# Optimization experiments

Measured on AMD Instinct MI355X. Metric: run time of the kernel, lower is better.

## Reference

```python
import jax, jax.numpy as jnp
import numpy as np

NUM_NODES = 512
HEADS = 4
IN_F = 256
OUT_F = 128
EPS = 1e-5


def _layernorm(x, g, b):
    mu = jnp.mean(x, axis=-1, keepdims=True)
    var = jnp.mean(jnp.square(x - mu), axis=-1, keepdims=True)
    return (x - mu) * jax.lax.rsqrt(var + EPS) * g + b


def setup_inputs() -> dict:
    key = jax.random.key(0)
    ks = jax.random.split(key, 16)
    N = 32 * NUM_NODES
    E = 262144
    s = 0.05
    return {
        "x": jax.random.normal(ks[0], (N, IN_F), jnp.float32),
        "edge_index": jax.random.randint(ks[1], (2, E), 0, N, jnp.int64),
        "W_l": jax.random.normal(ks[2], (IN_F, HEADS * OUT_F), jnp.float32) * s,
        "W_r": jax.random.normal(ks[3], (IN_F, HEADS * OUT_F), jnp.float32) * s,
        "att": jax.random.normal(ks[4], (HEADS, OUT_F), jnp.float32) * s,
        "gat_bias": jnp.zeros((OUT_F,), jnp.float32),
        "gat_gamma": jnp.ones((OUT_F,), jnp.float32),
        "gat_beta": jnp.zeros((OUT_F,), jnp.float32),
        "cnn_W": jax.random.normal(ks[5], (IN_F, OUT_F), jnp.float32) * s,
        "cnn_b": jnp.zeros((OUT_F,), jnp.float32),
        "conv_W": jax.random.normal(ks[6], (OUT_F, OUT_F, 7), jnp.float32) * s,
        "conv_b": jnp.zeros((OUT_F,), jnp.float32),
        "cnn_gamma": jnp.ones((OUT_F,), jnp.float32),
        "cnn_beta": jnp.zeros((OUT_F,), jnp.float32),
        "res_W": jax.random.normal(ks[7], (IN_F, OUT_F), jnp.float32) * s,
        "res_b": jnp.zeros((OUT_F,), jnp.float32),
        "fuse_gamma": jnp.ones((OUT_F,), jnp.float32),
        "fuse_beta": jnp.zeros((OUT_F,), jnp.float32),
    }


def reference(x, edge_index, W_l, W_r, att, gat_bias, gat_gamma, gat_beta,
              cnn_W, cnn_b, conv_W, conv_b, cnn_gamma, cnn_beta,
              res_W, res_b, fuse_gamma, fuse_beta):
    N = x.shape[0]
    B = N // NUM_NODES
    # --- GATv2 branch (add self-loops like PyG default) ---
    loop = jnp.arange(N, dtype=edge_index.dtype)
    src = jnp.concatenate([edge_index[0], loop])
    dst = jnp.concatenate([edge_index[1], loop])
    x_l = (x @ W_l).reshape(N, HEADS, OUT_F)
    x_r = (x @ W_r).reshape(N, HEADS, OUT_F)
    e = x_l[src] + x_r[dst]                      # [E+N, H, F]
    e = jnp.where(e > 0, e, 0.2 * e)             # leaky_relu, slope 0.2
    score = jnp.einsum('ehf,hf->eh', e, att)     # [E+N, H]
    m = jax.ops.segment_max(score, dst, num_segments=N)
    ex = jnp.exp(score - m[dst])
    denom = jax.ops.segment_sum(ex, dst, num_segments=N)
    alpha = ex / denom[dst]
    agg = jax.ops.segment_sum(alpha[:, :, None] * x_l[src], dst, num_segments=N)
    h_gat = jnp.mean(agg, axis=1) + gat_bias     # concat=False -> head mean
    h_gat = jnp.where(h_gat > 0, h_gat, 0.01 * h_gat)  # nn.LeakyReLU default
    h_gat = _layernorm(h_gat, gat_gamma, gat_beta)
    # --- CNN branch ---
    xc = x @ cnn_W + cnn_b                       # [N, F]
    xc = xc.reshape(B, NUM_NODES, OUT_F).transpose(0, 2, 1)  # [B, F, L]
    hc = jax.lax.conv_general_dilated(xc, conv_W, window_strides=(1,),
                                      padding=[(3, 3)],
                                      dimension_numbers=('NCW', 'OIW', 'NCW'))
    hc = hc + conv_b[None, :, None]
    hc = hc.transpose(0, 2, 1).reshape(N, OUT_F)
    hc = jax.nn.relu(hc)
    hc = _layernorm(hc, cnn_gamma, cnn_beta)
    # --- fuse + residual ---
    h = h_gat + hc + (x @ res_W + res_b)
    return _layernorm(h, fuse_gamma, fuse_beta)
```

## Files before the change

kernel.cpp:

```cpp
#include <hip/hip_runtime.h>
#include <hip/hip_bf16.h>
#include <math.h>

#define IN_F 256
#define OUT_F 128
#define HEADS 4
#define HF 512
#define NCAT 1280

typedef __hip_bfloat16 bf16;
typedef unsigned short ushort_t;

using bf16x8 = __attribute__((ext_vector_type(8))) short;
using f32x4  = __attribute__((ext_vector_type(4))) float;

__device__ __forceinline__ float bflo(unsigned u) { return __uint_as_float(u << 16); }
__device__ __forceinline__ float bfhi(unsigned u) { return __uint_as_float(u & 0xffff0000u); }
__device__ __forceinline__ float bf2f(ushort_t u) { return __uint_as_float((unsigned)u << 16); }
__device__ __forceinline__ ushort_t f2bf(float f) {
    __hip_bfloat16 h = __float2bfloat16(f);
    return *reinterpret_cast<ushort_t*>(&h);
}

template <int CTRL>
__device__ __forceinline__ float dpp_add(float s) {
    int t = __builtin_amdgcn_update_dpp(0, __float_as_int(s), CTRL, 0xf, 0xf, true);
    return s + __int_as_float(t);
}
__device__ __forceinline__ float rowsum16(float s) {
    s = dpp_add<0x121>(s);
    s = dpp_add<0x122>(s);
    s = dpp_add<0x124>(s);
    s = dpp_add<0x128>(s);
    return s;
}

__global__ __launch_bounds__(256) void cvt_x_kernel(
    const float* __restrict__ x, ushort_t* __restrict__ xb, int n) {
    int i = (blockIdx.x * 256 + threadIdx.x) * 8;
    if (i >= n) return;
    float4 a = *(const float4*)(x + i);
    float4 b = *(const float4*)(x + i + 4);
    uint4 o;
    o.x = f2bf(a.x) | ((unsigned)f2bf(a.y) << 16);
    o.y = f2bf(a.z) | ((unsigned)f2bf(a.w) << 16);
    o.z = f2bf(b.x) | ((unsigned)f2bf(b.y) << 16);
    o.w = f2bf(b.z) | ((unsigned)f2bf(b.w) << 16);
    *(uint4*)(xb + i) = o;
}

__global__ __launch_bounds__(256) void build_weights_kernel(
    const float* __restrict__ Wl, const float* __restrict__ Wr,
    const float* __restrict__ Wc, const float* __restrict__ Wres,
    const float* __restrict__ Wconv,
    ushort_t* __restrict__ Wt, ushort_t* __restrict__ Wt2) {
    int idx = blockIdx.x * 256 + threadIdx.x;
    if (idx < NCAT * 256) {
        int n = idx >> 8, k = idx & 255;
        float v;
        if (n < 512)       v = Wl[(size_t)k * 512 + n];
        else if (n < 1024) v = Wr[(size_t)k * 512 + (n - 512)];
        else if (n < 1152) v = Wc[(size_t)k * 128 + (n - 1024)];
        else               v = Wres[(size_t)k * 128 + (n - 1152)];
        Wt[idx] = f2bf(v);
    } else {
        int j = idx - NCAT * 256;
        if (j < 7 * 128 * 128) {
            int k = j >> 14, o = (j >> 7) & 127, i = j & 127;
            Wt2[j] = f2bf(Wconv[((size_t)o * 128 + i) * 7 + k]);
        }
    }
}

__global__ __launch_bounds__(256) void mfma_gemm(
    const ushort_t* __restrict__ A,
    const ushort_t* __restrict__ Wt,
    ushort_t* __restrict__ xlb, ushort_t* __restrict__ xrb,
    ushort_t* __restrict__ xcb, ushort_t* __restrict__ resb,
    int M) {
    __shared__ ushort_t As[128][40];
    __shared__ ushort_t Bs[128][40];
    int tid = threadIdx.x;
    int lane = tid & 63, wid = tid >> 6;
    int wr = (wid >> 1) * 64, wc = (wid & 1) * 64;
    int brow = blockIdx.y * 128, bcol = blockIdx.x * 128;
    f32x4 acc[4][4] = {};
    int kb = (lane >> 4) * 8;
    int rl = lane & 15;
    for (int k0 = 0; k0 < 256; k0 += 32) {
        #pragma unroll
        for (int i = 0; i < 2; ++i) {
            int idx = tid + 256 * i;
            int row = idx >> 2, seg = idx & 3;
            *(uint4*)&As[row][seg * 8] =
                *(const uint4*)(A + (size_t)(brow + row) * 256 + k0 + seg * 8);
            *(uint4*)&Bs[row][seg * 8] =
                *(const uint4*)(Wt + (size_t)(bcol + row) * 256 + k0 + seg * 8);
        }
        __syncthreads();
        bf16x8 af[4], bfr[4];
        #pragma unroll
        for (int m = 0; m < 4; ++m) af[m] = *(const bf16x8*)&As[wr + m * 16 + rl][kb];
        #pragma unroll
        for (int n = 0; n < 4; ++n) bfr[n] = *(const bf16x8*)&Bs[wc + n * 16 + rl][kb];
        #pragma unroll
        for (int m = 0; m < 4; ++m)
            #pragma unroll
            for (int n = 0; n < 4; ++n)
                acc[m][n] = __builtin_amdgcn_mfma_f32_16x16x32_bf16(
                    af[m], bfr[n], acc[m][n], 0, 0, 0);
        __syncthreads();
    }
    ushort_t* dstp; int cstride, cb;
    if (bcol < 512)       { dstp = xlb;  cstride = 512; cb = bcol; }
    else if (bcol < 1024) { dstp = xrb;  cstride = 512; cb = bcol - 512; }
    else if (bcol < 1152) { dstp = xcb;  cstride = 128; cb = bcol - 1024; }
    else                  { dstp = resb; cstride = 128; cb = bcol - 1152; }
    int rowb = (lane >> 4) * 4;
    #pragma unroll
    for (int m = 0; m < 4; ++m)
        #pragma unroll
        for (int n = 0; n < 4; ++n) {
            int col = cb + wc + n * 16 + rl;
            #pragma unroll
            for (int q = 0; q < 4; ++q) {
                int row = brow + wr + m * 16 + rowb + q;
                dstp[(size_t)row * cstride + col] = f2bf(acc[m][n][q]);
            }
        }
}

__global__ __launch_bounds__(256) void conv_mfma(
    const ushort_t* __restrict__ xcb, const float* __restrict__ cnn_b,
    const ushort_t* __restrict__ Wt2, float* __restrict__ hc) {
    __shared__ ushort_t As[70][136];
    __shared__ ushort_t Bs[128][136];
    int tid = threadIdx.x;
    int lane = tid & 63, wid = tid >> 6;
    int wr = (wid >> 1) * 32, wc = (wid & 1) * 64;
    int b = blockIdx.y, l0 = blockIdx.x * 64;
    for (int u = tid; u < 70 * 16; u += 256) {
        int r = u >> 4, seg = u & 15;
        int l = l0 - 3 + r;
        uint4 o4 = make_uint4(0, 0, 0, 0);
        if (l >= 0 && l < 512) {
            uint4 v = *(const uint4*)(xcb + (size_t)(b * 512 + l) * 128 + seg * 8);
            float4 b0 = *(const float4*)(cnn_b + seg * 8);
            float4 b1 = *(const float4*)(cnn_b + seg * 8 + 4);
            o4.x = f2bf(bflo(v.x) + b0.x) | ((unsigned)f2bf(bfhi(v.x) + b0.y) << 16);
            o4.y = f2bf(bflo(v.y) + b0.z) | ((unsigned)f2bf(bfhi(v.y) + b0.w) << 16);
            o4.z = f2bf(bflo(v.z) + b1.x) | ((unsigned)f2bf(bfhi(v.z) + b1.y) << 16);
            o4.w = f2bf(bflo(v.w) + b1.z) | ((unsigned)f2bf(bfhi(v.w) + b1.w) << 16);
        }
        *(uint4*)&As[r][seg * 8] = o4;
    }
    f32x4 acc[2][4] = {};
    int rl = lane & 15, kb = (lane >> 4) * 8;
    for (int k = 0; k < 7; ++k) {
        __syncthreads();
        for (int u = tid; u < 128 * 16; u += 256) {
            int r = u >> 4, seg = u & 15;
            *(uint4*)&Bs[r][seg * 8] =
                *(const uint4*)(Wt2 + ((size_t)(k * 128 + r)) * 128 + seg * 8);
        }
        __syncthreads();
        #pragma unroll
        for (int kk = 0; kk < 4; ++kk) {
            bf16x8 af[2], bfr[4];
            af[0] = *(const bf16x8*)&As[wr + 0  + rl + k][kk * 32 + kb];
            af[1] = *(const bf16x8*)&As[wr + 16 + rl + k][kk * 32 + kb];
            #pragma unroll
            for (int n = 0; n < 4; ++n)
                bfr[n] = *(const bf16x8*)&Bs[wc + n * 16 + rl][kk * 32 + kb];
            #pragma unroll
            for (int m = 0; m < 2; ++m)
                #pragma unroll
                for (int n = 0; n < 4; ++n)
                    acc[m][n] = __builtin_amdgcn_mfma_f32_16x16x32_bf16(
                        af[m], bfr[n], acc[m][n], 0, 0, 0);
        }
    }
    int rowb = (lane >> 4) * 4;
    #pragma unroll
    for (int m = 0; m < 2; ++m)
        #pragma unroll
        for (int n = 0; n < 4; ++n) {
            int col = wc + n * 16 + rl;
            #pragma unroll
            for (int q = 0; q < 4; ++q) {
                int l = l0 + wr + m * 16 + rowb + q;
                hc[(size_t)(b * 512 + l) * 128 + col] = acc[m][n][q];
            }
        }
}

__global__ __launch_bounds__(256) void hist_kernel(
    const int* __restrict__ ei, int* __restrict__ counts, int E) {
    int e = blockIdx.x * 256 + threadIdx.x;
    if (e < E) atomicAdd(&counts[ei[E + e]], 1);
}

__global__ __launch_bounds__(1024) void scan_kernel(
    const int* __restrict__ counts, int* __restrict__ offs,
    int* __restrict__ cursor, int N) {
    __shared__ int wsum[16];
    int t = threadIdx.x;
    int lane = t & 63, w = t >> 6;
    int base = t * 16;
    int local[16], s = 0;
    #pragma unroll
    for (int i = 0; i < 16; ++i) {
        int v = (base + i < N) ? counts[base + i] : 0;
        local[i] = v; s += v;
    }
    int sc = s;
    #pragma unroll
    for (int off = 1; off < 64; off <<= 1) {
        int v = __shfl_up(sc, off);
        if (lane >= off) sc += v;
    }
    if (lane == 63) wsum[w] = sc;
    __syncthreads();
    if (w == 0 && lane < 16) {
        int v = wsum[lane];
        int scv = v;
        #pragma unroll
        for (int off = 1; off < 16; off <<= 1) {
            int u = __shfl_up(scv, off);
            if (lane >= off) scv += u;
        }
        wsum[lane] = scv - v;
    }
    __syncthreads();
    int run = wsum[w] + sc - s;
    #pragma unroll
    for (int i = 0; i < 16; ++i) {
        if (base + i < N) { offs[base + i] = run; cursor[base + i] = run; }
        run += local[i];
    }
}

__global__ __launch_bounds__(256) void scatter_kernel(
    const int* __restrict__ ei, int* __restrict__ cursor,
    int* __restrict__ srcs, int E) {
    int e = blockIdx.x * 256 + threadIdx.x;
    if (e < E) {
        int d = ei[E + e];
        int p = atomicAdd(&cursor[d], 1);
        srcs[p] = ei[e];
    }
}

__global__ __launch_bounds__(256) void gat_fused_kernel(
    const ushort_t* __restrict__ xlb, const ushort_t* __restrict__ xrb,
    const int* __restrict__ srcs, const int* __restrict__ offs,
    const float* __restrict__ att, const float* __restrict__ gat_bias,
    const float* __restrict__ gat_gamma, const float* __restrict__ gat_beta,
    float* __restrict__ hgat_ln, int E, int N) {
    int wid = (blockIdx.x * 256 + threadIdx.x) >> 6;
    int lane = threadIdx.x & 63;
    if (wid >= N) return;
    int d = wid;
    const uint4 rv = ((const uint4*)(xrb + (size_t)d * HF))[lane];
    float xr8[8];
    xr8[0] = bflo(rv.x); xr8[1] = bfhi(rv.x);
    xr8[2] = bflo(rv.y); xr8[3] = bfhi(rv.y);
    xr8[4] = bflo(rv.z); xr8[5] = bfhi(rv.z);
    xr8[6] = bflo(rv.w); xr8[7] = bfhi(rv.w);
    const float4 a0 = ((const float4*)att)[lane * 2];
    const float4 a1 = ((const float4*)att)[lane * 2 + 1];
    const float aw[8] = {a0.x, a0.y, a0.z, a0.w, a1.x, a1.y, a1.z, a1.w};
    float acc[8] = {};
    float dn = 0.f;

    auto process = [&](uint4 lv) {
        float xl8[8];
        xl8[0] = bflo(lv.x); xl8[1] = bfhi(lv.x);
        xl8[2] = bflo(lv.y); xl8[3] = bfhi(lv.y);
        xl8[4] = bflo(lv.z); xl8[5] = bfhi(lv.z);
        xl8[6] = bflo(lv.w); xl8[7] = bfhi(lv.w);
        float s = 0.f;
        #pragma unroll
        for (int j = 0; j < 8; ++j) {
            float v = xl8[j] + xr8[j];
            v = v > 0.f ? v : 0.2f * v;
            s = fmaf(v, aw[j], s);
        }
        s = rowsum16(s);
        float ex = __expf(s);
        dn += ex;
        #pragma unroll
        for (int j = 0; j < 8; ++j) acc[j] = fmaf(ex, xl8[j], acc[j]);
    };

    process(((const uint4*)(xlb + (size_t)d * HF))[lane]);

    int start = offs[d];
    int end = (d == N - 1) ? E : offs[d + 1];
    int p = start;
    for (; p + 3 < end; p += 4) {
        int s0 = srcs[p], s1 = srcs[p + 1], s2 = srcs[p + 2], s3 = srcs[p + 3];
        uint4 l0 = ((const uint4*)(xlb + (size_t)s0 * HF))[lane];
        uint4 l1 = ((const uint4*)(xlb + (size_t)s1 * HF))[lane];
        uint4 l2 = ((const uint4*)(xlb + (size_t)s2 * HF))[lane];
        uint4 l3 = ((const uint4*)(xlb + (size_t)s3 * HF))[lane];
        process(l0); process(l1); process(l2); process(l3);
    }
    for (; p < end; ++p)
        process(((const uint4*)(xlb + (size_t)srcs[p] * HF))[lane]);

    float inv = 1.f / dn;
    float v[8];
    #pragma unroll
    for (int j = 0; j < 8; ++j) {
        float t2 = acc[j] * inv;
        t2 += __shfl_xor(t2, 16);
        t2 += __shfl_xor(t2, 32);
        v[j] = t2;
    }
    int h = lane >> 4;
    int col = (lane & 15) * 8 + 2 * h;
    float g0 = 0.25f * v[2 * h]     + gat_bias[col];
    float g1 = 0.25f * v[2 * h + 1] + gat_bias[col + 1];
    g0 = g0 > 0.f ? g0 : 0.01f * g0;
    g1 = g1 > 0.f ? g1 : 0.01f * g1;
    float s = g0 + g1;
    #pragma unroll
    for (int off = 32; off; off >>= 1) s += __shfl_xor(s, off);
    float mu = s * (1.f / 128.f);
    float d0 = g0 - mu, d1 = g1 - mu;
    float vs = d0 * d0 + d1 * d1;
    #pragma unroll
    for (int off = 32; off; off >>= 1) vs += __shfl_xor(vs, off);
    float rinv = rsqrtf(vs * (1.f / 128.f) + 1e-5f);
    hgat_ln[(size_t)d * 128 + col]     = d0 * rinv * gat_gamma[col]     + gat_beta[col];
    hgat_ln[(size_t)d * 128 + col + 1] = d1 * rinv * gat_gamma[col + 1] + gat_beta[col + 1];
}

__global__ __launch_bounds__(256) void final_ln_kernel(
    const float* __restrict__ hgat_ln, const float* __restrict__ hc,
    const ushort_t* __restrict__ resb, const float* __restrict__ conv_b,
    const float* __restrict__ cnn_gamma, const float* __restrict__ cnn_beta,
    const float* __restrict__ res_b, const float* __restrict__ fuse_gamma,
    const float* __restrict__ fuse_beta, float* __restrict__ out, int N) {
    int wid = (blockIdx.x * 256 + threadIdx.x) >> 6;
    int lane = threadIdx.x & 63;
    if (wid >= N) return;
    size_t base = (size_t)wid * 128;
    float h0 = fmaxf(hc[base + lane]      + conv_b[lane], 0.f);
    float h1 = fmaxf(hc[base + lane + 64] + conv_b[lane + 64], 0.f);
    float s = h0 + h1;
    #pragma unroll
    for (int off = 32; off; off >>= 1) s += __shfl_xor(s, off);
    float mu = s * (1.f / 128.f);
    float d0 = h0 - mu, d1 = h1 - mu;
    float vs = d0 * d0 + d1 * d1;
    #pragma unroll
    for (int off = 32; off; off >>= 1) vs += __shfl_xor(vs, off);
    float inv = rsqrtf(vs * (1.f / 128.f) + 1e-5f);
    float hcn0 = d0 * inv * cnn_gamma[lane]      + cnn_beta[lane];
    float hcn1 = d1 * inv * cnn_gamma[lane + 64] + cnn_beta[lane + 64];
    float v0 = hgat_ln[base + lane]      + hcn0
             + bf2f(resb[base + lane])      + res_b[lane];
    float v1 = hgat_ln[base + lane + 64] + hcn1
             + bf2f(resb[base + lane + 64]) + res_b[lane + 64];
    s = v0 + v1;
    #pragma unroll
    for (int off = 32; off; off >>= 1) s += __shfl_xor(s, off);
    mu = s * (1.f / 128.f);
    d0 = v0 - mu; d1 = v1 - mu;
    vs = d0 * d0 + d1 * d1;
    #pragma unroll
    for (int off = 32; off; off >>= 1) vs += __shfl_xor(vs, off);
    inv = rsqrtf(vs * (1.f / 128.f) + 1e-5f);
    out[base + lane]      = d0 * inv * fuse_gamma[lane]      + fuse_beta[lane];
    out[base + lane + 64] = d1 * inv * fuse_gamma[lane + 64] + fuse_beta[lane + 64];
}

extern "C" void kernel_launch(void* const* d_in, const int* in_sizes, int n_in,
                              void* d_out, int out_size, void* d_ws, size_t ws_size,
                              hipStream_t stream) {
    const float* x         = (const float*)d_in[0];
    const int*   ei        = (const int*)d_in[1];
    const float* W_l       = (const float*)d_in[2];
    const float* W_r       = (const float*)d_in[3];
    const float* att       = (const float*)d_in[4];
    const float* gat_bias  = (const float*)d_in[5];
    const float* gat_gamma = (const float*)d_in[6];
    const float* gat_beta  = (const float*)d_in[7];
    const float* cnn_W     = (const float*)d_in[8];
    const float* cnn_b     = (const float*)d_in[9];
    const float* conv_W    = (const float*)d_in[10];
    const float* conv_b    = (const float*)d_in[11];
    const float* cnn_gamma = (const float*)d_in[12];
    const float* cnn_beta  = (const float*)d_in[13];
    const float* res_W     = (const float*)d_in[14];
    const float* res_b     = (const float*)d_in[15];
    const float* fuse_gamma= (const float*)d_in[16];
    const float* fuse_beta = (const float*)d_in[17];

    int N = in_sizes[0] / IN_F;
    int E = in_sizes[1] / 2;

    char* ws = (char*)d_ws;
    size_t off = 0;
    ushort_t* xb     = (ushort_t*)(ws + off); off += (size_t)N * IN_F * 2;
    ushort_t* Wt     = (ushort_t*)(ws + off); off += (size_t)NCAT * IN_F * 2;
    ushort_t* Wt2    = (ushort_t*)(ws + off); off += (size_t)7 * 128 * 128 * 2;
    ushort_t* xlb    = (ushort_t*)(ws + off); off += (size_t)N * HF * 2;
    ushort_t* xrb    = (ushort_t*)(ws + off); off += (size_t)N * HF * 2;
    ushort_t* xcb    = (ushort_t*)(ws + off); off += (size_t)N * 128 * 2;
    ushort_t* resb   = (ushort_t*)(ws + off); off += (size_t)N * 128 * 2;
    int*  counts     = (int*)(ws + off);  off += (size_t)N * 4;
    int*  offs       = (int*)(ws + off);  off += (size_t)N * 4;
    int*  cursor     = (int*)(ws + off);  off += (size_t)N * 4;
    int*  srcs       = (int*)(ws + off);  off += (size_t)E * 4;
    float* hgat_ln   = (float*)(ws + off); off += (size_t)N * 128 * 4;
    float* hc        = (float*)(ws + off); off += (size_t)N * 128 * 4;

    hipMemsetAsync(counts, 0, (size_t)N * 4, stream);

    dim3 blk(256);
    hist_kernel<<<(E + 255) / 256, blk, 0, stream>>>(ei, counts, E);
    scan_kernel<<<1, 1024, 0, stream>>>(counts, offs, cursor, N);
    scatter_kernel<<<(E + 255) / 256, blk, 0, stream>>>(ei, cursor, srcs, E);

    cvt_x_kernel<<<(N * IN_F / 8 + 255) / 256, blk, 0, stream>>>(x, xb, N * IN_F);
    build_weights_kernel<<<(NCAT * 256 + 7 * 128 * 128 + 255) / 256, blk, 0, stream>>>(
        W_l, W_r, cnn_W, res_W, conv_W, Wt, Wt2);

    mfma_gemm<<<dim3(NCAT / 128, N / 128), blk, 0, stream>>>(
        xb, Wt, xlb, xrb, xcb, resb, N);

    gat_fused_kernel<<<(N + 3) / 4, blk, 0, stream>>>(
        xlb, xrb, srcs, offs, att, gat_bias, gat_gamma, gat_beta, hgat_ln, E, N);

    conv_mfma<<<dim3(8, 32), blk, 0, stream>>>(xcb, cnn_b, Wt2, hc);

    final_ln_kernel<<<(N + 3) / 4, blk, 0, stream>>>(
        hgat_ln, hc, resb, conv_b, cnn_gamma, cnn_beta, res_b,
        fuse_gamma, fuse_beta, (float*)d_out, N);
}
```

Before: 160.2 us.

## Merge prep kernels and fuse conv with final layernorm epilogue

Three small prep kernels (x bf16 conversion, weight packing, edge-degree histogram) become one launch that dispatches on block index. The conv MFMA kernel now uses 32-row tiles and applies bias, ReLU, both layernorms and the residual add in its epilogue via shared memory, so the fp32 hc intermediate and the separate final kernel are gone. Leaky-ReLU in the GAT score is rewritten as 0.6*v + 0.4*|v| to avoid a branch. The conv grid doubles and the weight tile is reloaded more often per output row, which costs some reuse in exchange for fewer launches and less global traffic.

```diff
diff --git a/kernel.cpp b/kernel.cpp
--- a/kernel.cpp
+++ b/kernel.cpp
@@ -35,40 +35,46 @@
     return s;
 }
 
-__global__ __launch_bounds__(256) void cvt_x_kernel(
-    const float* __restrict__ x, ushort_t* __restrict__ xb, int n) {
-    int i = (blockIdx.x * 256 + threadIdx.x) * 8;
-    if (i >= n) return;
-    float4 a = *(const float4*)(x + i);
-    float4 b = *(const float4*)(x + i + 4);
-    uint4 o;
-    o.x = f2bf(a.x) | ((unsigned)f2bf(a.y) << 16);
-    o.y = f2bf(a.z) | ((unsigned)f2bf(a.w) << 16);
-    o.z = f2bf(b.x) | ((unsigned)f2bf(b.y) << 16);
-    o.w = f2bf(b.z) | ((unsigned)f2bf(b.w) << 16);
-    *(uint4*)(xb + i) = o;
-}
-
-__global__ __launch_bounds__(256) void build_weights_kernel(
+__global__ __launch_bounds__(256) void prep_kernel(
+    const float* __restrict__ x, ushort_t* __restrict__ xb, int n_cvt,
     const float* __restrict__ Wl, const float* __restrict__ Wr,
     const float* __restrict__ Wc, const float* __restrict__ Wres,
     const float* __restrict__ Wconv,
-    ushort_t* __restrict__ Wt, ushort_t* __restrict__ Wt2) {
-    int idx = blockIdx.x * 256 + threadIdx.x;
-    if (idx < NCAT * 256) {
-        int n = idx >> 8, k = idx & 255;
-        float v;
-        if (n < 512)       v = Wl[(size_t)k * 512 + n];
-        else if (n < 1024) v = Wr[(size_t)k * 512 + (n - 512)];
-        else if (n < 1152) v = Wc[(size_t)k * 128 + (n - 1024)];
-        else               v = Wres[(size_t)k * 128 + (n - 1152)];
-        Wt[idx] = f2bf(v);
+    ushort_t* __restrict__ Wt, ushort_t* __restrict__ Wt2,
+    const int* __restrict__ ei, int* __restrict__ counts, int E,
+    int g1, int g2) {
+    int b = blockIdx.x;
+    if (b < g1) {
+        int i = (b * 256 + threadIdx.x) * 8;
+        if (i >= n_cvt) return;
+        float4 a = *(const float4*)(x + i);
+        float4 c = *(const float4*)(x + i + 4);
+        uint4 o;
+        o.x = f2bf(a.x) | ((unsigned)f2bf(a.y) << 16);
+        o.y = f2bf(a.z) | ((unsigned)f2bf(a.w) << 16);
+        o.z = f2bf(c.x) | ((unsigned)f2bf(c.y) << 16);
+        o.w = f2bf(c.z) | ((unsigned)f2bf(c.w) << 16);
+        *(uint4*)(xb + i) = o;
+    } else if (b < g2) {
+        int idx = (b - g1) * 256 + threadIdx.x;
+        if (idx < NCAT * 256) {
+            int n = idx >> 8, k = idx & 255;
+            float v;
+            if (n < 512)       v = Wl[(size_t)k * 512 + n];
+            else if (n < 1024) v = Wr[(size_t)k * 512 + (n - 512)];
+            else if (n < 1152) v = Wc[(size_t)k * 128 + (n - 1024)];
+            else               v = Wres[(size_t)k * 128 + (n - 1152)];
+            Wt[idx] = f2bf(v);
+        } else {
+            int j = idx - NCAT * 256;
+            if (j < 7 * 128 * 128) {
+                int k = j >> 14, o = (j >> 7) & 127, i = j & 127;
+                Wt2[j] = f2bf(Wconv[((size_t)o * 128 + i) * 7 + k]);
+            }
+        }
     } else {
-        int j = idx - NCAT * 256;
-        if (j < 7 * 128 * 128) {
-            int k = j >> 14, o = (j >> 7) & 127, i = j & 127;
-            Wt2[j] = f2bf(Wconv[((size_t)o * 128 + i) * 7 + k]);
-        }
+        int e = (b - g2) * 256 + threadIdx.x;
+        if (e < E) atomicAdd(&counts[ei[E + e]], 1);
     }
 }
 
@@ -128,76 +134,6 @@
                 dstp[(size_t)row * cstride + col] = f2bf(acc[m][n][q]);
             }
         }
-}
-
-__global__ __launch_bounds__(256) void conv_mfma(
-    const ushort_t* __restrict__ xcb, const float* __restrict__ cnn_b,
-    const ushort_t* __restrict__ Wt2, float* __restrict__ hc) {
-    __shared__ ushort_t As[70][136];
-    __shared__ ushort_t Bs[128][136];
-    int tid = threadIdx.x;
-    int lane = tid & 63, wid = tid >> 6;
-    int wr = (wid >> 1) * 32, wc = (wid & 1) * 64;
-    int b = blockIdx.y, l0 = blockIdx.x * 64;
-    for (int u = tid; u < 70 * 16; u += 256) {
-        int r = u >> 4, seg = u & 15;
-        int l = l0 - 3 + r;
-        uint4 o4 = make_uint4(0, 0, 0, 0);
-        if (l >= 0 && l < 512) {
-            uint4 v = *(const uint4*)(xcb + (size_t)(b * 512 + l) * 128 + seg * 8);
-            float4 b0 = *(const float4*)(cnn_b + seg * 8);
-            float4 b1 = *(const float4*)(cnn_b + seg * 8 + 4);
-            o4.x = f2bf(bflo(v.x) + b0.x) | ((unsigned)f2bf(bfhi(v.x) + b0.y) << 16);
-            o4.y = f2bf(bflo(v.y) + b0.z) | ((unsigned)f2bf(bfhi(v.y) + b0.w) << 16);
-            o4.z = f2bf(bflo(v.z) + b1.x) | ((unsigned)f2bf(bfhi(v.z) + b1.y) << 16);
-            o4.w = f2bf(bflo(v.w) + b1.z) | ((unsigned)f2bf(bfhi(v.w) + b1.w) << 16);
-        }
-        *(uint4*)&As[r][seg * 8] = o4;
-    }
-    f32x4 acc[2][4] = {};
-    int rl = lane & 15, kb = (lane >> 4) * 8;
-    for (int k = 0; k < 7; ++k) {
-        __syncthreads();
-        for (int u = tid; u < 128 * 16; u += 256) {
-            int r = u >> 4, seg = u & 15;
-            *(uint4*)&Bs[r][seg * 8] =
-                *(const uint4*)(Wt2 + ((size_t)(k * 128 + r)) * 128 + seg * 8);
-        }
-        __syncthreads();
-        #pragma unroll
-        for (int kk = 0; kk < 4; ++kk) {
-            bf16x8 af[2], bfr[4];
-            af[0] = *(const bf16x8*)&As[wr + 0  + rl + k][kk * 32 + kb];
-            af[1] = *(const bf16x8*)&As[wr + 16 + rl + k][kk * 32 + kb];
-            #pragma unroll
-            for (int n = 0; n < 4; ++n)
-                bfr[n] = *(const bf16x8*)&Bs[wc + n * 16 + rl][kk * 32 + kb];
-            #pragma unroll
-            for (int m = 0; m < 2; ++m)
-                #pragma unroll
-                for (int n = 0; n < 4; ++n)
-                    acc[m][n] = __builtin_amdgcn_mfma_f32_16x16x32_bf16(
-                        af[m], bfr[n], acc[m][n], 0, 0, 0);
-        }
-    }
-    int rowb = (lane >> 4) * 4;
-    #pragma unroll
-    for (int m = 0; m < 2; ++m)
-        #pragma unroll
-        for (int n = 0; n < 4; ++n) {
-            int col = wc + n * 16 + rl;
-            #pragma unroll
-            for (int q = 0; q < 4; ++q) {
-                int l = l0 + wr + m * 16 + rowb + q;
-                hc[(size_t)(b * 512 + l) * 128 + col] = acc[m][n][q];
-            }
-        }
-}
-
-__global__ __launch_bounds__(256) void hist_kernel(
-    const int* __restrict__ ei, int* __restrict__ counts, int E) {
-    int e = blockIdx.x * 256 + threadIdx.x;
-    if (e < E) atomicAdd(&counts[ei[E + e]], 1);
 }
 
 __global__ __launch_bounds__(1024) void scan_kernel(
@@ -279,13 +215,14 @@
         xl8[2] = bflo(lv.y); xl8[3] = bfhi(lv.y);
         xl8[4] = bflo(lv.z); xl8[5] = bfhi(lv.z);
         xl8[6] = bflo(lv.w); xl8[7] = bfhi(lv.w);
-        float s = 0.f;
+        float s1 = 0.f, s2 = 0.f;
         #pragma unroll
         for (int j = 0; j < 8; ++j) {
             float v = xl8[j] + xr8[j];
-            v = v > 0.f ? v : 0.2f * v;
-            s = fmaf(v, aw[j], s);
-        }
+            s1 = fmaf(v, aw[j], s1);
+            s2 = fmaf(fabsf(v), aw[j], s2);
+        }
+        float s = fmaf(0.6f, s1, 0.4f * s2);
         s = rowsum16(s);
         float ex = __expf(s);
         dn += ex;
@@ -337,44 +274,101 @@
     hgat_ln[(size_t)d * 128 + col + 1] = d1 * rinv * gat_gamma[col + 1] + gat_beta[col + 1];
 }
 
-__global__ __launch_bounds__(256) void final_ln_kernel(
-    const float* __restrict__ hgat_ln, const float* __restrict__ hc,
-    const ushort_t* __restrict__ resb, const float* __restrict__ conv_b,
+__global__ __launch_bounds__(256) void conv_fuse_kernel(
+    const ushort_t* __restrict__ xcb, const float* __restrict__ cnn_b,
+    const ushort_t* __restrict__ Wt2,
+    const float* __restrict__ hgat_ln, const ushort_t* __restrict__ resb,
+    const float* __restrict__ conv_b,
     const float* __restrict__ cnn_gamma, const float* __restrict__ cnn_beta,
-    const float* __restrict__ res_b, const float* __restrict__ fuse_gamma,
-    const float* __restrict__ fuse_beta, float* __restrict__ out, int N) {
-    int wid = (blockIdx.x * 256 + threadIdx.x) >> 6;
-    int lane = threadIdx.x & 63;
-    if (wid >= N) return;
-    size_t base = (size_t)wid * 128;
-    float h0 = fmaxf(hc[base + lane]      + conv_b[lane], 0.f);
-    float h1 = fmaxf(hc[base + lane + 64] + conv_b[lane + 64], 0.f);
-    float s = h0 + h1;
-    #pragma unroll
-    for (int off = 32; off; off >>= 1) s += __shfl_xor(s, off);
-    float mu = s * (1.f / 128.f);
-    float d0 = h0 - mu, d1 = h1 - mu;
-    float vs = d0 * d0 + d1 * d1;
-    #pragma unroll
-    for (int off = 32; off; off >>= 1) vs += __shfl_xor(vs, off);
-    float inv = rsqrtf(vs * (1.f / 128.f) + 1e-5f);
-    float hcn0 = d0 * inv * cnn_gamma[lane]      + cnn_beta[lane];
-    float hcn1 = d1 * inv * cnn_gamma[lane + 64] + cnn_beta[lane + 64];
-    float v0 = hgat_ln[base + lane]      + hcn0
-             + bf2f(resb[base + lane])      + res_b[lane];
-    float v1 = hgat_ln[base + lane + 64] + hcn1
-             + bf2f(resb[base + lane + 64]) + res_b[lane + 64];
-    s = v0 + v1;
-    #pragma unroll
-    for (int off = 32; off; off >>= 1) s += __shfl_xor(s, off);
-    mu = s * (1.f / 128.f);
-    d0 = v0 - mu; d1 = v1 - mu;
-    vs = d0 * d0 + d1 * d1;
-    #pragma unroll
-    for (int off = 32; off; off >>= 1) vs += __shfl_xor(vs, off);
-    inv = rsqrtf(vs * (1.f / 128.f) + 1e-5f);
-    out[base + lane]      = d0 * inv * fuse_gamma[lane]      + fuse_beta[lane];
-    out[base + lane + 64] = d1 * inv * fuse_gamma[lane + 64] + fuse_beta[lane + 64];
+    const float* __restrict__ res_b,
+    const float* __restrict__ fuse_gamma, const float* __restrict__ fuse_beta,
+    float* __restrict__ out) {
+    __shared__ ushort_t As[38][136];
+    __shared__ ushort_t Bs[128][136];
+    __shared__ float hbuf[32][129];
+    int tid = threadIdx.x;
+    int lane = tid & 63, wid = tid >> 6;
+    int wr = (wid >> 1) * 16, wc = (wid & 1) * 64;
+    int b = blockIdx.y, l0 = blockIdx.x * 32;
+    for (int u = tid; u < 38 * 16; u += 256) {
+        int r = u >> 4, seg = u & 15;
+        int l = l0 - 3 + r;
+        uint4 o4 = make_uint4(0, 0, 0, 0);
+        if (l >= 0 && l < 512) {
+            uint4 v = *(const uint4*)(xcb + (size_t)(b * 512 + l) * 128 + seg * 8);
+            float4 b0 = *(const float4*)(cnn_b + seg * 8);
+            float4 b1 = *(const float4*)(cnn_b + seg * 8 + 4);
+            o4.x = f2bf(bflo(v.x) + b0.x) | ((unsigned)f2bf(bfhi(v.x) + b0.y) << 16);
+            o4.y = f2bf(bflo(v.y) + b0.z) | ((unsigned)f2bf(bfhi(v.y) + b0.w) << 16);
+            o4.z = f2bf(bflo(v.z) + b1.x) | ((unsigned)f2bf(bfhi(v.z) + b1.y) << 16);
+            o4.w = f2bf(bflo(v.w) + b1.z) | ((unsigned)f2bf(bfhi(v.w) + b1.w) << 16);
+        }
+        *(uint4*)&As[r][seg * 8] = o4;
+    }
+    f32x4 acc[4] = {};
+    int rl = lane & 15, kb = (lane >> 4) * 8;
+    for (int k = 0; k < 7; ++k) {
+        __syncthreads();
+        for (int u = tid; u < 128 * 16; u += 256) {
+            int r = u >> 4, seg = u & 15;
+            *(uint4*)&Bs[r][seg * 8] =
+                *(const uint4*)(Wt2 + ((size_t)(k * 128 + r)) * 128 + seg * 8);
+        }
+        __syncthreads();
+        #pragma unroll
+        for (int kk = 0; kk < 4; ++kk) {
+            bf16x8 af = *(const bf16x8*)&As[wr + rl + k][kk * 32 + kb];
+            #pragma unroll
+            for (int n = 0; n < 4; ++n) {
+                bf16x8 bfr = *(const bf16x8*)&Bs[wc + n * 16 + rl][kk * 32 + kb];
+                acc[n] = __builtin_amdgcn_mfma_f32_16x16x32_bf16(af, bfr, acc[n], 0, 0, 0);
+            }
+        }
+    }
+    __syncthreads();
+    int rowb = (lane >> 4) * 4;
+    #pragma unroll
+    for (int n = 0; n < 4; ++n) {
+        int col = wc + n * 16 + rl;
+        float cb = conv_b[col];
+        #pragma unroll
+        for (int q = 0; q < 4; ++q) {
+            int r = wr + rowb + q;
+            hbuf[r][col] = fmaxf(acc[n][q] + cb, 0.f);
+        }
+    }
+    __syncthreads();
+    for (int r = wid * 8; r < wid * 8 + 8; ++r) {
+        int grow = b * 512 + l0 + r;
+        float h0 = hbuf[r][lane], h1 = hbuf[r][lane + 64];
+        float s = h0 + h1;
+        #pragma unroll
+        for (int off = 32; off; off >>= 1) s += __shfl_xor(s, off);
+        float mu = s * (1.f / 128.f);
+        float d0 = h0 - mu, d1 = h1 - mu;
+        float vs = d0 * d0 + d1 * d1;
+        #pragma unroll
+        for (int off = 32; off; off >>= 1) vs += __shfl_xor(vs, off);
+        float inv = rsqrtf(vs * (1.f / 128.f) + 1e-5f);
+        float hcn0 = d0 * inv * cnn_gamma[lane]      + cnn_beta[lane];
+        float hcn1 = d1 * inv * cnn_gamma[lane + 64] + cnn_beta[lane + 64];
+        size_t base = (size_t)grow * 128;
+        float v0 = hgat_ln[base + lane]      + hcn0
+                 + bf2f(resb[base + lane])      + res_b[lane];
+        float v1 = hgat_ln[base + lane + 64] + hcn1
+                 + bf2f(resb[base + lane + 64]) + res_b[lane + 64];
+        s = v0 + v1;
+        #pragma unroll
+        for (int off = 32; off; off >>= 1) s += __shfl_xor(s, off);
+        mu = s * (1.f / 128.f);
+        d0 = v0 - mu; d1 = v1 - mu;
+        vs = d0 * d0 + d1 * d1;
+        #pragma unroll
+        for (int off = 32; off; off >>= 1) vs += __shfl_xor(vs, off);
+        inv = rsqrtf(vs * (1.f / 128.f) + 1e-5f);
+        out[base + lane]      = d0 * inv * fuse_gamma[lane]      + fuse_beta[lane];
+        out[base + lane + 64] = d1 * inv * fuse_gamma[lane + 64] + fuse_beta[lane + 64];
+    }
 }
 
 extern "C" void kernel_launch(void* const* d_in, const int* in_sizes, int n_in,
@@ -416,28 +410,27 @@
     int*  cursor     = (int*)(ws + off);  off += (size_t)N * 4;
     int*  srcs       = (int*)(ws + off);  off += (size_t)E * 4;
     float* hgat_ln   = (float*)(ws + off); off += (size_t)N * 128 * 4;
-    float* hc        = (float*)(ws + off); off += (size_t)N * 128 * 4;
 
     hipMemsetAsync(counts, 0, (size_t)N * 4, stream);
 
     dim3 blk(256);
-    hist_kernel<<<(E + 255) / 256, blk, 0, stream>>>(ei, counts, E);
+    int n_cvt = N * IN_F;
+    int g1 = (n_cvt / 8 + 255) / 256;
+    int g2 = g1 + (NCAT * 256 + 7 * 128 * 128 + 255) / 256;
+    int g3 = g2 + (E + 255) / 256;
+    prep_kernel<<<g3, blk, 0, stream>>>(x, xb, n_cvt,
+        W_l, W_r, cnn_W, res_W, conv_W, Wt, Wt2, ei, counts, E, g1, g2);
+
     scan_kernel<<<1, 1024, 0, stream>>>(counts, offs, cursor, N);
     scatter_kernel<<<(E + 255) / 256, blk, 0, stream>>>(ei, cursor, srcs, E);
 
-    cvt_x_kernel<<<(N * IN_F / 8 + 255) / 256, blk, 0, stream>>>(x, xb, N * IN_F);
-    build_weights_kernel<<<(NCAT * 256 + 7 * 128 * 128 + 255) / 256, blk, 0, stream>>>(
-        W_l, W_r, cnn_W, res_W, conv_W, Wt, Wt2);
-
     mfma_gemm<<<dim3(NCAT / 128, N / 128), blk, 0, stream>>>(
         xb, Wt, xlb, xrb, xcb, resb, N);
 
     gat_fused_kernel<<<(N + 3) / 4, blk, 0, stream>>>(
         xlb, xrb, srcs, offs, att, gat_bias, gat_gamma, gat_beta, hgat_ln, E, N);
 
-    conv_mfma<<<dim3(8, 32), blk, 0, stream>>>(xcb, cnn_b, Wt2, hc);
-
-    final_ln_kernel<<<(N + 3) / 4, blk, 0, stream>>>(
-        hgat_ln, hc, resb, conv_b, cnn_gamma, cnn_beta, res_b,
-        fuse_gamma, fuse_beta, (float*)d_out, N);
-}
+    conv_fuse_kernel<<<dim3(16, 32), blk, 0, stream>>>(
+        xcb, cnn_b, Wt2, hgat_ln, resb, conv_b, cnn_gamma, cnn_beta,
+        res_b, fuse_gamma, fuse_beta, (float*)d_out);
+}
```

Measured after the change: 150.8 us. 5.9% less time.
